# Kernel optimization log

Measured on AMD Instinct MI355X. Metric: run time of the kernel, lower is better.

The kernel has to match this reference:

```python
import jax, jax.numpy as jnp
import numpy as np

N_NODES = 100000
N_EDGES = 1600000
N_GRAPHS = 2048
IN0 = 33
H = 100
NUM_TASKS = 1
BN_EPS = 1e-5


def _gcn_layer(x, W, b, row, col, norm, n):
    # x: [N, Cin] -> [N, Cout]; GCNConv: symmetric-normalized aggregation of x @ W, plus bias
    xw = x @ W                                   # [N, Cout]
    msg = xw[row] * norm[:, None]                # [E+N, Cout] gathered + scaled messages
    out = jax.ops.segment_sum(msg, col, num_segments=n)
    return out + b


def _bn_eval(h, gamma, beta, mean, var):
    return (h - mean) * jax.lax.rsqrt(var + BN_EPS) * gamma + beta


def setup_inputs() -> dict:
    key = jax.random.key(0)
    ks = jax.random.split(key, 16)
    x = jax.random.normal(ks[0], (N_NODES, IN0), dtype=jnp.float32)
    edge_index = jax.random.randint(ks[1], (2, N_EDGES), 0, N_NODES, dtype=jnp.int64)
    batch = jnp.sort(jax.random.randint(ks[2], (N_NODES,), 0, N_GRAPHS, dtype=jnp.int64))
    # Xavier-uniform linear weights (as in _initialize_weights), zero biases
    def xav(k, fan_in, fan_out):
        lim = np.sqrt(6.0 / (fan_in + fan_out))
        return jax.random.uniform(k, (fan_in, fan_out), jnp.float32, -lim, lim)
    W0 = xav(ks[3], IN0, H)                      # layer 0: 33 -> 100
    Ws = jnp.stack([xav(ks[4 + i], H, H) for i in range(3)])  # layers 1..3: 100 -> 100
    biases = jnp.zeros((4, H), jnp.float32)
    gamma = 1.0 + 0.1 * jax.random.normal(ks[7], (4, H), jnp.float32)
    beta = 0.1 * jax.random.normal(ks[8], (4, H), jnp.float32)
    bn_mean = 0.1 * jax.random.normal(ks[9], (4, H), jnp.float32)
    bn_var = 1.0 + 0.1 * jax.random.uniform(ks[10], (4, H), jnp.float32)
    head_W = xav(ks[11], H, NUM_TASKS)
    head_b = jnp.zeros((NUM_TASKS,), jnp.float32)
    return {"x": x, "edge_index": edge_index, "batch": batch, "W0": W0, "Ws": Ws,
            "biases": biases, "gamma": gamma, "beta": beta, "bn_mean": bn_mean,
            "bn_var": bn_var, "head_W": head_W, "head_b": head_b}


def reference(x, edge_index, batch, W0, Ws, biases, gamma, beta, bn_mean, bn_var, head_W, head_b):
    n = x.shape[0]
    loop = jnp.arange(n, dtype=edge_index.dtype)
    row = jnp.concatenate([edge_index[0], loop])     # sources (+ self loops)
    col = jnp.concatenate([edge_index[1], loop])     # destinations (+ self loops)
    deg = jax.ops.segment_sum(jnp.ones_like(col, dtype=x.dtype), col, num_segments=n)
    dis = jnp.where(deg > 0, jax.lax.rsqrt(jnp.maximum(deg, 1.0)), 0.0)
    norm = dis[row] * dis[col]                       # [E+N] symmetric GCN normalization
    h = x
    for l in range(4):
        W = W0 if l == 0 else Ws[l - 1]
        h = _gcn_layer(h, W, biases[l], row, col, norm, n)
        h = _bn_eval(h, gamma[l], beta[l], bn_mean[l], bn_var[l])
        if l < 3:
            h = jax.nn.relu(h)
        # dropout: identity in eval mode
    g = jax.ops.segment_sum(h, batch, num_segments=N_GRAPHS)  # global_add_pool [G, H]
    out = g @ head_W + head_b
    return jnp.where(out >= 0, out, 0.1 * out)       # LeakyReLU(0.1)
```

## Files before the change

kernel.cpp:

```cpp
#include <hip/hip_runtime.h>
#include <hip/hip_fp16.h>

#define H100 100
#define BN_EPS 1e-5f
#define MAXD 64

typedef _Float16 h2t __attribute__((ext_vector_type(2)));

__device__ __forceinline__ float dot2f(h2t a, h2t b, float c) {
#if defined(__has_builtin) && __has_builtin(__builtin_amdgcn_fdot2)
    return __builtin_amdgcn_fdot2(a, b, c, false);
#else
    return c + (float)a.x * (float)b.x + (float)a.y * (float)b.y;
#endif
}

__device__ __forceinline__ float4 h4tof4(const uint2 u) {
    const __half2 h0 = *reinterpret_cast<const __half2*>(&u.x);
    const __half2 h1 = *reinterpret_cast<const __half2*>(&u.y);
    const float2 f0 = __half22float2(h0);
    const float2 f1 = __half22float2(h1);
    return make_float4(f0.x, f0.y, f1.x, f1.y);
}
__device__ __forceinline__ uint2 f4toh4(const float4 v) {
    __half2 h0 = __float22half2_rn(make_float2(v.x, v.y));
    __half2 h1 = __float22half2_rn(make_float2(v.z, v.w));
    uint2 u;
    u.x = *reinterpret_cast<const unsigned int*>(&h0);
    u.y = *reinterpret_cast<const unsigned int*>(&h1);
    return u;
}
__device__ __forceinline__ void f4p(float4& a, const float4 b) {
    a.x += b.x; a.y += b.y; a.z += b.z; a.w += b.w;
}

__global__ __launch_bounds__(256) void init_kernel(
    int* __restrict__ cnt, int n, int nbc,
    const float* __restrict__ b, const float* __restrict__ gamma,
    const float* __restrict__ beta, const float* __restrict__ mean,
    const float* __restrict__ var, const float* __restrict__ W0,
    const float* __restrict__ Ws, const float* __restrict__ headW,
    float* __restrict__ sarr, float* __restrict__ tarr,
    h2t* __restrict__ W0p2, h2t* __restrict__ W1p2, h2t* __restrict__ W2p2,
    float* __restrict__ wp, float* __restrict__ c3,
    float* __restrict__ gacc, int G)
{
    const int t = threadIdx.x;
    if (blockIdx.x < nbc) {
        int gid = blockIdx.x * 256 + t;
        if (gid < n) cnt[gid] = 0;
        return;
    }
    if (blockIdx.x == nbc) {
        __shared__ float ws_[H100];
        const float* W3 = Ws + 2 * H100 * H100;
        for (int idx = t; idx < 4 * H100; idx += 256) {
            float s = gamma[idx] * rsqrtf(var[idx] + BN_EPS);
            sarr[idx] = s;
            tarr[idx] = (b[idx] - mean[idx]) * s + beta[idx];
        }
        __syncthreads();
        if (t < H100) ws_[t] = sarr[3 * H100 + t] * headW[t];
        __syncthreads();
        if (t < H100) {
            float acc = 0.f;
            for (int c = 0; c < H100; ++c) acc += W3[t * H100 + c] * ws_[c];
            wp[t] = acc;
        }
        if (t == 0) {
            float acc = 0.f;
            for (int c = 0; c < H100; ++c) acc += tarr[3 * H100 + c] * headW[c];
            *c3 = acc;
        }
        return;
    }
    int idx = (blockIdx.x - nbc - 1) * 256 + t;
    if (idx < 1800) {
        int k2 = idx / 100, c = idx - k2 * 100;
        int k0 = 2 * k2, k1 = 2 * k2 + 1;
        float v0 = (k0 < 33) ? W0[k0 * H100 + c] : 0.f;
        float v1 = (k1 < 33) ? W0[k1 * H100 + c] : 0.f;
        h2t p; p.x = (_Float16)v0; p.y = (_Float16)v1;
        W0p2[idx] = p;
    } else if (idx < 6800) {
        int j = idx - 1800;
        int k2 = j / 100, c = j - k2 * 100;
        h2t p;
        p.x = (_Float16)Ws[(2 * k2) * H100 + c];
        p.y = (_Float16)Ws[(2 * k2 + 1) * H100 + c];
        W1p2[j] = p;
    } else if (idx < 12000) {
        int j = idx - 6800;
        int k2 = j / 104, c = j - k2 * 104;
        const float* W2 = Ws + H100 * H100;
        h2t p; p.x = (_Float16)0.f; p.y = (_Float16)0.f;
        if (c < H100) {
            p.x = (_Float16)W2[(2 * k2) * H100 + c];
            p.y = (_Float16)W2[(2 * k2 + 1) * H100 + c];
        }
        W2p2[j] = p;
    } else {
        int g = idx - 12000;
        if (g < G) gacc[g] = 0.f;
    }
}

__global__ __launch_bounds__(256) void fill_kernel(
    const int* __restrict__ row, const int* __restrict__ col,
    int* __restrict__ cnt, int* __restrict__ srcidx, int E)
{
    const int e0 = blockIdx.x * 2048 + threadIdx.x;
    int c[8], r[8], s[8];
    bool v[8];
    #pragma unroll
    for (int k = 0; k < 8; ++k) {
        const int e = e0 + k * 256;
        v[k] = (e < E);
        c[k] = v[k] ? col[e] : 0;
        r[k] = v[k] ? row[e] : 0;
    }
    #pragma unroll
    for (int k = 0; k < 8; ++k)
        if (v[k]) s[k] = atomicAdd(&cnt[c[k]], 1);
    #pragma unroll
    for (int k = 0; k < 8; ++k)
        if (v[k] && s[k] < MAXD) srcidx[(size_t)c[k] * MAXD + s[k]] = r[k];
}

__global__ __launch_bounds__(256) void dis_kernel(const int* __restrict__ cnt,
                                                  float* __restrict__ dis, int n) {
    int gid = blockIdx.x * 256 + threadIdx.x;
    if (gid < n) dis[gid] = rsqrtf((float)(cnt[gid] + 1));
}

__global__ __launch_bounds__(256) void xpad_kernel(
    const float* __restrict__ x, const float* __restrict__ dis,
    uint2* __restrict__ xts, int n)
{
    int tt = blockIdx.x * 256 + threadIdx.x;
    int node = tt / 9;
    if (node >= n) return;
    int q = tt - node * 9;
    const float dn = dis[node];
    float v[4];
    #pragma unroll
    for (int j = 0; j < 4; ++j) {
        int c = q * 4 + j;
        v[j] = (c < 33) ? x[node * 33 + c] * dn : 0.f;
    }
    xts[node * 9 + q] = f4toh4(make_float4(v[0], v[1], v[2], v[3]));
}

__global__ __launch_bounds__(256) void gather33_kernel(
    const int* __restrict__ cnt, const int* __restrict__ srcidx,
    const uint2* __restrict__ xts, const float* __restrict__ dis,
    float4* __restrict__ agg0, int n)
{
    const int t = blockIdx.x * 256 + threadIdx.x;
    const int node = t / 9;
    if (node >= n) return;
    const int q = t - node * 9;
    const float dn = dis[node];
    const int* __restrict__ sp = srcidx + (size_t)node * MAXD;
    const int kd = min(cnt[node], MAXD);

    float4 a0 = h4tof4(xts[node * 9 + q]);
    float4 a1 = make_float4(0.f, 0.f, 0.f, 0.f);
    int i = 0;
    for (; i + 3 < kd; i += 4) {
        const uint2 u0 = xts[sp[i] * 9 + q];
        const uint2 u1 = xts[sp[i + 1] * 9 + q];
        const uint2 u2 = xts[sp[i + 2] * 9 + q];
        const uint2 u3 = xts[sp[i + 3] * 9 + q];
        f4p(a0, h4tof4(u0)); f4p(a1, h4tof4(u1));
        f4p(a0, h4tof4(u2)); f4p(a1, h4tof4(u3));
    }
    for (; i < kd; ++i) f4p(a1, h4tof4(xts[sp[i] * 9 + q]));
    agg0[node * 9 + q] = make_float4((a0.x + a1.x) * dn, (a0.y + a1.y) * dn,
                                     (a0.z + a1.z) * dn, (a0.w + a1.w) * dn);
}

__global__ __launch_bounds__(256) void gemm_fused36_kernel(
    const float* __restrict__ agg0,
    const h2t* __restrict__ W0p2, const h2t* __restrict__ W1p2,
    const float* __restrict__ dis,
    const float* __restrict__ sarr0, const float* __restrict__ tarr0,
    uint2* __restrict__ z1h, int n)
{
    __shared__ h2t Wl[50 * H100];
    __shared__ h2t Uh[50 * 68];
    const int tid = threadIdx.x;
    const int node0 = blockIdx.x * 64;

    for (int idx = tid; idx < 64 * 18; idx += 256) {
        int r = idx / 18;
        int k2 = idx - r * 18;
        int node = node0 + r;
        h2t p; p.x = (_Float16)0.f; p.y = (_Float16)0.f;
        if (node < n) {
            const float2 ag = *reinterpret_cast<const float2*>(&agg0[node * 36 + 2 * k2]);
            p.x = (_Float16)ag.x; p.y = (_Float16)ag.y;
        }
        Uh[k2 * 68 + r] = p;
    }
    for (int idx = tid; idx < 450; idx += 256)
        reinterpret_cast<uint4*>(Wl)[idx] = reinterpret_cast<const uint4*>(W0p2)[idx];
    __syncthreads();

    const int tx = tid & 15;
    const int ty = tid >> 4;
    float acc0[4][4] = {{0.f}};
    float acc1[4][4] = {{0.f}};

    #pragma unroll 3
    for (int k2 = 0; k2 < 18; ++k2) {
        const uint4 av = *reinterpret_cast<const uint4*>(&Uh[k2 * 68 + ty * 4]);
        const h2t* a2 = reinterpret_cast<const h2t*>(&av);
        const uint4 w0v = *reinterpret_cast<const uint4*>(&Wl[k2 * H100 + tx * 4]);
        const h2t* w0 = reinterpret_cast<const h2t*>(&w0v);
        #pragma unroll
        for (int ni = 0; ni < 4; ++ni)
            #pragma unroll
            for (int ci = 0; ci < 4; ++ci)
                acc0[ni][ci] = dot2f(a2[ni], w0[ci], acc0[ni][ci]);
        if (tx < 9) {
            const uint4 w1v = *reinterpret_cast<const uint4*>(&Wl[k2 * H100 + 64 + tx * 4]);
            const h2t* w1 = reinterpret_cast<const h2t*>(&w1v);
            #pragma unroll
            for (int ni = 0; ni < 4; ++ni)
                #pragma unroll
                for (int ci = 0; ci < 4; ++ci)
                    acc1[ni][ci] = dot2f(a2[ni], w1[ci], acc1[ni][ci]);
        }
    }
    __syncthreads();

    {
        const float4 s0 = *reinterpret_cast<const float4*>(&sarr0[tx * 4]);
        const float4 t0 = *reinterpret_cast<const float4*>(&tarr0[tx * 4]);
        #pragma unroll
        for (int ni = 0; ni < 4; ++ni) {
            const int r = ty * 4 + ni;
            float h0 = fmaxf(acc0[ni][0] * s0.x + t0.x, 0.f);
            float h1 = fmaxf(acc0[ni][1] * s0.y + t0.y, 0.f);
            float hh2 = fmaxf(acc0[ni][2] * s0.z + t0.z, 0.f);
            float h3 = fmaxf(acc0[ni][3] * s0.w + t0.w, 0.f);
            h2t p0; p0.x = (_Float16)h0; p0.y = (_Float16)h1;
            h2t p1; p1.x = (_Float16)hh2; p1.y = (_Float16)h3;
            Uh[(tx * 2) * 68 + r] = p0;
            Uh[(tx * 2 + 1) * 68 + r] = p1;
        }
        if (tx < 9) {
            const float4 s1 = *reinterpret_cast<const float4*>(&sarr0[64 + tx * 4]);
            const float4 t1 = *reinterpret_cast<const float4*>(&tarr0[64 + tx * 4]);
            #pragma unroll
            for (int ni = 0; ni < 4; ++ni) {
                const int r = ty * 4 + ni;
                float h0 = fmaxf(acc1[ni][0] * s1.x + t1.x, 0.f);
                float h1 = fmaxf(acc1[ni][1] * s1.y + t1.y, 0.f);
                float hh2 = fmaxf(acc1[ni][2] * s1.z + t1.z, 0.f);
                float h3 = fmaxf(acc1[ni][3] * s1.w + t1.w, 0.f);
                h2t p0; p0.x = (_Float16)h0; p0.y = (_Float16)h1;
                h2t p1; p1.x = (_Float16)hh2; p1.y = (_Float16)h3;
                Uh[(32 + tx * 2) * 68 + r] = p0;
                Uh[(32 + tx * 2 + 1) * 68 + r] = p1;
            }
        }
    }
    for (int idx = tid; idx < 1250; idx += 256)
        reinterpret_cast<uint4*>(Wl)[idx] = reinterpret_cast<const uint4*>(W1p2)[idx];
    __syncthreads();

    float bcc0[4][4] = {{0.f}};
    float bcc1[4][4] = {{0.f}};
    #pragma unroll 5
    for (int k2 = 0; k2 < 50; ++k2) {
        const uint4 av = *reinterpret_cast<const uint4*>(&Uh[k2 * 68 + ty * 4]);
        const h2t* a2 = reinterpret_cast<const h2t*>(&av);
        const uint4 w0v = *reinterpret_cast<const uint4*>(&Wl[k2 * H100 + tx * 4]);
        const h2t* w0 = reinterpret_cast<const h2t*>(&w0v);
        #pragma unroll
        for (int ni = 0; ni < 4; ++ni)
            #pragma unroll
            for (int ci = 0; ci < 4; ++ci)
                bcc0[ni][ci] = dot2f(a2[ni], w0[ci], bcc0[ni][ci]);
        if (tx < 9) {
            const uint4 w1v = *reinterpret_cast<const uint4*>(&Wl[k2 * H100 + 64 + tx * 4]);
            const h2t* w1 = reinterpret_cast<const h2t*>(&w1v);
            #pragma unroll
            for (int ni = 0; ni < 4; ++ni)
                #pragma unroll
                for (int ci = 0; ci < 4; ++ci)
                    bcc1[ni][ci] = dot2f(a2[ni], w1[ci], bcc1[ni][ci]);
        }
    }

    #pragma unroll
    for (int ni = 0; ni < 4; ++ni) {
        const int node = node0 + ty * 4 + ni;
        if (node >= n) continue;
        const float d = dis[node];
        z1h[node * 25 + tx] = f4toh4(make_float4(
            bcc0[ni][0] * d, bcc0[ni][1] * d, bcc0[ni][2] * d, bcc0[ni][3] * d));
        if (tx < 9)
            z1h[node * 25 + 16 + tx] = f4toh4(make_float4(
                bcc1[ni][0] * d, bcc1[ni][1] * d, bcc1[ni][2] * d, bcc1[ni][3] * d));
    }
}

__global__ __launch_bounds__(512) void gather_gemm_kernel(
    const int* __restrict__ cnt, const int* __restrict__ srcidx,
    const uint2* __restrict__ z4, const float* __restrict__ dis,
    const float* __restrict__ sarr, const float* __restrict__ tarr,
    const h2t* __restrict__ W2p2, uint2* __restrict__ z2h, int n)
{
    __shared__ h2t Wl[50 * 104];
    __shared__ h2t hrow[20 * 52];
    const int tid = threadIdx.x;

    const int g = tid / 25;
    const int q = tid - g * 25;
    const bool act = (g < 20);
    const int node = blockIdx.x * 20 + g;
    const bool valid = act && (node < n);

    float4 a0 = make_float4(0.f, 0.f, 0.f, 0.f);
    float4 a1 = make_float4(0.f, 0.f, 0.f, 0.f);
    float dn = 0.f;
    if (valid) {
        a0 = h4tof4(z4[node * 25 + q]);
        dn = dis[node];
        const int* __restrict__ sp = srcidx + (size_t)node * MAXD;
        const int kd = min(cnt[node], MAXD);
        int i = 0;
        for (; i + 7 < kd; i += 8) {
            const uint2 u0 = z4[sp[i] * 25 + q];
            const uint2 u1 = z4[sp[i + 1] * 25 + q];
            const uint2 u2 = z4[sp[i + 2] * 25 + q];
            const uint2 u3 = z4[sp[i + 3] * 25 + q];
            const uint2 u4 = z4[sp[i + 4] * 25 + q];
            const uint2 u5 = z4[sp[i + 5] * 25 + q];
            const uint2 u6 = z4[sp[i + 6] * 25 + q];
            const uint2 u7 = z4[sp[i + 7] * 25 + q];
            f4p(a0, h4tof4(u0)); f4p(a1, h4tof4(u1));
            f4p(a0, h4tof4(u2)); f4p(a1, h4tof4(u3));
            f4p(a0, h4tof4(u4)); f4p(a1, h4tof4(u5));
            f4p(a0, h4tof4(u6)); f4p(a1, h4tof4(u7));
        }
        for (; i + 3 < kd; i += 4) {
            const uint2 u0 = z4[sp[i] * 25 + q];
            const uint2 u1 = z4[sp[i + 1] * 25 + q];
            const uint2 u2 = z4[sp[i + 2] * 25 + q];
            const uint2 u3 = z4[sp[i + 3] * 25 + q];
            f4p(a0, h4tof4(u0)); f4p(a1, h4tof4(u1));
            f4p(a0, h4tof4(u2)); f4p(a1, h4tof4(u3));
        }
        for (; i < kd; ++i) f4p(a1, h4tof4(z4[sp[i] * 25 + q]));
    }

    if (act) {
        const float4 s  = *reinterpret_cast<const float4*>(&sarr[q * 4]);
        const float4 tt = *reinterpret_cast<const float4*>(&tarr[q * 4]);
        float h0 = fmaxf((a0.x + a1.x) * dn * s.x + tt.x, 0.f);
        float h1 = fmaxf((a0.y + a1.y) * dn * s.y + tt.y, 0.f);
        float hh2 = fmaxf((a0.z + a1.z) * dn * s.z + tt.z, 0.f);
        float h3 = fmaxf((a0.w + a1.w) * dn * s.w + tt.w, 0.f);
        h2t p0; p0.x = (_Float16)h0; p0.y = (_Float16)h1;
        h2t p1; p1.x = (_Float16)hh2; p1.y = (_Float16)h3;
        hrow[g * 52 + q * 2]     = p0;
        hrow[g * 52 + q * 2 + 1] = p1;
    }

    for (int idx = tid; idx < 1300; idx += 512)
        reinterpret_cast<uint4*>(Wl)[idx] = reinterpret_cast<const uint4*>(W2p2)[idx];
    __syncthreads();

    if (valid) {
        float z0 = 0.f, zz1 = 0.f, z2v = 0.f, z3 = 0.f;
        const h2t* hp = &hrow[g * 52];
        #pragma unroll 5
        for (int k2 = 0; k2 < 50; ++k2) {
            const uint4 wv = *reinterpret_cast<const uint4*>(&Wl[k2 * 104 + q * 4]);
            const h2t* wh = reinterpret_cast<const h2t*>(&wv);
            const h2t hv = hp[k2];
            z0  = dot2f(hv, wh[0], z0);
            zz1 = dot2f(hv, wh[1], zz1);
            z2v = dot2f(hv, wh[2], z2v);
            z3  = dot2f(hv, wh[3], z3);
        }
        z2h[node * 25 + q] = f4toh4(make_float4(z0 * dn, zz1 * dn, z2v * dn, z3 * dn));
    }
}

__global__ __launch_bounds__(256) void gather100_head_kernel(
    const int* __restrict__ cnt, const int* __restrict__ srcidx,
    const uint2* __restrict__ z4, const float* __restrict__ dis,
    const float* __restrict__ sarr, const float* __restrict__ tarr,
    const float* __restrict__ wp, float* __restrict__ y, int n)
{
    const int tid = threadIdx.x;
    const int node = blockIdx.x * 10 + tid / 25;
    const int q = tid % 25;
    const bool valid = (tid < 250) && (node < n);

    float4 a0 = make_float4(0.f, 0.f, 0.f, 0.f);
    float4 a1 = make_float4(0.f, 0.f, 0.f, 0.f);
    float dn = 0.f;
    if (valid) {
        a0 = h4tof4(z4[node * 25 + q]);
        dn = dis[node];
        const int* __restrict__ sp = srcidx + (size_t)node * MAXD;
        const int kd = min(cnt[node], MAXD);
        int i = 0;
        for (; i + 7 < kd; i += 8) {
            const uint2 u0 = z4[sp[i] * 25 + q];
            const uint2 u1 = z4[sp[i + 1] * 25 + q];
            const uint2 u2 = z4[sp[i + 2] * 25 + q];
            const uint2 u3 = z4[sp[i + 3] * 25 + q];
            const uint2 u4 = z4[sp[i + 4] * 25 + q];
            const uint2 u5 = z4[sp[i + 5] * 25 + q];
            const uint2 u6 = z4[sp[i + 6] * 25 + q];
            const uint2 u7 = z4[sp[i + 7] * 25 + q];
            f4p(a0, h4tof4(u0)); f4p(a1, h4tof4(u1));
            f4p(a0, h4tof4(u2)); f4p(a1, h4tof4(u3));
            f4p(a0, h4tof4(u4)); f4p(a1, h4tof4(u5));
            f4p(a0, h4tof4(u6)); f4p(a1, h4tof4(u7));
        }
        for (; i + 3 < kd; i += 4) {
            const uint2 u0 = z4[sp[i] * 25 + q];
            const uint2 u1 = z4[sp[i + 1] * 25 + q];
            const uint2 u2 = z4[sp[i + 2] * 25 + q];
            const uint2 u3 = z4[sp[i + 3] * 25 + q];
            f4p(a0, h4tof4(u0)); f4p(a1, h4tof4(u1));
            f4p(a0, h4tof4(u2)); f4p(a1, h4tof4(u3));
        }
        for (; i < kd; ++i) f4p(a1, h4tof4(z4[sp[i] * 25 + q]));
    }

    const float4 s  = *reinterpret_cast<const float4*>(&sarr[q * 4]);
    const float4 tt = *reinterpret_cast<const float4*>(&tarr[q * 4]);
    const float4 w  = *reinterpret_cast<const float4*>(&wp[q * 4]);
    float hv0 = fmaxf((a0.x + a1.x) * dn * s.x + tt.x, 0.f);
    float hv1 = fmaxf((a0.y + a1.y) * dn * s.y + tt.y, 0.f);
    float hv2 = fmaxf((a0.z + a1.z) * dn * s.z + tt.z, 0.f);
    float hv3 = fmaxf((a0.w + a1.w) * dn * s.w + tt.w, 0.f);
    float partial = hv0 * w.x + hv1 * w.y + hv2 * w.z + hv3 * w.w;

    __shared__ float red[256];
    red[tid] = valid ? partial : 0.f;
    __syncthreads();
    if (valid && q == 0) {
        float sum = 0.f;
        #pragma unroll
        for (int j = 0; j < 25; ++j) sum += red[tid + j];
        y[node] = sum * dn;
    }
}

__global__ __launch_bounds__(256) void gather_scalar_kernel(
    const int* __restrict__ cnt, const int* __restrict__ srcidx,
    const float* __restrict__ y, const float* __restrict__ dis,
    const float* __restrict__ c3, const int* __restrict__ batch,
    float* __restrict__ gacc, int n)
{
    const int node = blockIdx.x * 256 + threadIdx.x;
    if (node >= n) return;
    float acc = y[node];
    float accb = 0.f;
    const int* __restrict__ sp = srcidx + (size_t)node * MAXD;
    const int kd = min(cnt[node], MAXD);
    int i = 0;
    for (; i + 7 < kd; i += 8) {
        acc  += (y[sp[i]]     + y[sp[i + 1]]) + (y[sp[i + 2]] + y[sp[i + 3]]);
        accb += (y[sp[i + 4]] + y[sp[i + 5]]) + (y[sp[i + 6]] + y[sp[i + 7]]);
    }
    for (; i + 3 < kd; i += 4)
        acc += (y[sp[i]] + y[sp[i + 1]]) + (y[sp[i + 2]] + y[sp[i + 3]]);
    for (; i < kd; ++i) acc += y[sp[i]];
    unsafeAtomicAdd(&gacc[batch[node]], dis[node] * (acc + accb) + c3[0]);
}

__global__ __launch_bounds__(256) void finish_kernel(const float* __restrict__ gacc,
                                                     const float* __restrict__ hb,
                                                     float* __restrict__ out, int G) {
    int g = blockIdx.x * 256 + threadIdx.x;
    if (g >= G) return;
    float o = gacc[g] + hb[0];
    out[g] = (o >= 0.f) ? o : 0.1f * o;
}

extern "C" void kernel_launch(void* const* d_in, const int* in_sizes, int n_in,
                              void* d_out, int out_size, void* d_ws, size_t ws_size,
                              hipStream_t stream) {
    const float* x       = (const float*)d_in[0];
    const int*   ei      = (const int*)d_in[1];
    const int*   batch   = (const int*)d_in[2];
    const float* W0      = (const float*)d_in[3];
    const float* Ws      = (const float*)d_in[4];
    const float* biases  = (const float*)d_in[5];
    const float* gamma   = (const float*)d_in[6];
    const float* beta    = (const float*)d_in[7];
    const float* bn_mean = (const float*)d_in[8];
    const float* bn_var  = (const float*)d_in[9];
    const float* headW   = (const float*)d_in[10];
    const float* headb   = (const float*)d_in[11];
    float* out = (float*)d_out;

    const int N = in_sizes[2];
    const int E = in_sizes[1] / 2;
    const int G = out_size;
    const int* row  = ei;
    const int* colp = ei + E;

    char* ws = (char*)d_ws;
    size_t off = 0;
    auto carve = [&](size_t bytes) -> void* {
        void* p = (void*)(ws + off);
        off += (bytes + 255) & ~(size_t)255;
        return p;
    };
    float*  dis    = (float*)carve((size_t)N * 4);
    uint2*  xts    = (uint2*)carve((size_t)N * 9 * 8);
    float4* agg0   = (float4*)carve((size_t)N * 9 * 16);
    uint2*  bufA   = (uint2*)carve((size_t)N * 25 * 8);
    uint2*  bufB   = (uint2*)carve((size_t)N * 25 * 8);
    float*  y      = (float*)carve((size_t)N * 4);
    int*    cnt    = (int*)carve((size_t)N * 4);
    int*    srcidx = (int*)carve((size_t)N * MAXD * 4);
    float*  sarr   = (float*)carve(4 * H100 * 4);
    float*  tarr   = (float*)carve(4 * H100 * 4);
    float*  wp     = (float*)carve(H100 * 4);
    float*  c3     = (float*)carve(256);
    h2t*    W0p2   = (h2t*)carve(1800 * 4);
    h2t*    W1p2   = (h2t*)carve(5000 * 4);
    h2t*    W2p2   = (h2t*)carve(5200 * 4);
    float*  gacc   = (float*)carve((size_t)G * 4);

    const int nb_n   = (N + 255) / 256;
    const int nb_g   = (N + 63) / 64;
    const int nb_9   = (N * 9 + 255) / 256;
    const int nb_ga  = (N + 9) / 10;
    const int nb_gg  = (N + 19) / 20;
    const int nb_f   = (E + 2047) / 2048;
    const int nb_pad = (12000 + G + 255) / 256;

    init_kernel<<<nb_n + 1 + nb_pad, 256, 0, stream>>>(
        cnt, N, nb_n,
        biases, gamma, beta, bn_mean, bn_var, W0,
        Ws, headW, sarr, tarr, W0p2, W1p2, W2p2, wp, c3, gacc, G);
    fill_kernel<<<nb_f, 256, 0, stream>>>(row, colp, cnt, srcidx, E);
    dis_kernel<<<nb_n, 256, 0, stream>>>(cnt, dis, N);
    xpad_kernel<<<nb_9, 256, 0, stream>>>(x, dis, xts, N);

    gather33_kernel<<<nb_9, 256, 0, stream>>>(cnt, srcidx, xts, dis, agg0, N);
    gemm_fused36_kernel<<<nb_g, 256, 0, stream>>>((const float*)agg0, W0p2, W1p2, dis,
                                                  sarr, tarr, bufA, N);

    gather_gemm_kernel<<<nb_gg, 512, 0, stream>>>(cnt, srcidx, bufA, dis,
                                                  sarr + H100, tarr + H100,
                                                  W2p2, bufB, N);

    gather100_head_kernel<<<nb_ga, 256, 0, stream>>>(cnt, srcidx, bufB, dis,
                                                     sarr + 2 * H100, tarr + 2 * H100, wp, y, N);

    gather_scalar_kernel<<<nb_n, 256, 0, stream>>>(cnt, srcidx, y, dis, c3, batch, gacc, N);
    finish_kernel<<<(G + 255) / 256, 256, 0, stream>>>(gacc, headb, out, G);
}
```

Measured before the change: 450.0 us.

## Build CSR adjacency via two-pass bucketed binning with shared-memory atomics

```diff
diff --git a/kernel.cpp b/kernel.cpp
--- a/kernel.cpp
+++ b/kernel.cpp
@@ -4,6 +4,8 @@
 #define H100 100
 #define BN_EPS 1e-5f
 #define MAXD 64
+#define CSR_CAP 5120
+#define NB_MAX 1024
 
 typedef _Float16 h2t __attribute__((ext_vector_type(2)));
 
@@ -35,7 +37,6 @@
 }
 
 __global__ __launch_bounds__(256) void init_kernel(
-    int* __restrict__ cnt, int n, int nbc,
     const float* __restrict__ b, const float* __restrict__ gamma,
     const float* __restrict__ beta, const float* __restrict__ mean,
     const float* __restrict__ var, const float* __restrict__ W0,
@@ -43,15 +44,11 @@
     float* __restrict__ sarr, float* __restrict__ tarr,
     h2t* __restrict__ W0p2, h2t* __restrict__ W1p2, h2t* __restrict__ W2p2,
     float* __restrict__ wp, float* __restrict__ c3,
-    float* __restrict__ gacc, int G)
+    float* __restrict__ gacc, int G,
+    int* __restrict__ bucketCnt, int NB)
 {
     const int t = threadIdx.x;
-    if (blockIdx.x < nbc) {
-        int gid = blockIdx.x * 256 + t;
-        if (gid < n) cnt[gid] = 0;
-        return;
-    }
-    if (blockIdx.x == nbc) {
+    if (blockIdx.x == 0) {
         __shared__ float ws_[H100];
         const float* W3 = Ws + 2 * H100 * H100;
         for (int idx = t; idx < 4 * H100; idx += 256) {
@@ -74,7 +71,7 @@
         }
         return;
     }
-    int idx = (blockIdx.x - nbc - 1) * 256 + t;
+    int idx = (blockIdx.x - 1) * 256 + t;
     if (idx < 1800) {
         int k2 = idx / 100, c = idx - k2 * 100;
         int k0 = 2 * k2, k1 = 2 * k2 + 1;
@@ -102,35 +99,78 @@
     } else {
         int g = idx - 12000;
         if (g < G) gacc[g] = 0.f;
-    }
-}
-
-__global__ __launch_bounds__(256) void fill_kernel(
+        else if (g - G < NB) bucketCnt[g - G] = 0;
+    }
+}
+
+__global__ __launch_bounds__(512) void csr_p1_kernel(
     const int* __restrict__ row, const int* __restrict__ col,
-    int* __restrict__ cnt, int* __restrict__ srcidx, int E)
-{
-    const int e0 = blockIdx.x * 2048 + threadIdx.x;
-    int c[8], r[8], s[8];
+    int* __restrict__ bucketCnt, unsigned int* __restrict__ bucketBuf,
+    int E, int NB)
+{
+    __shared__ int hcnt[NB_MAX];
+    __shared__ int hbase[NB_MAX];
+    const int tid = threadIdx.x;
+    for (int j = tid; j < NB; j += 512) hcnt[j] = 0;
+    __syncthreads();
+
+    const int e0 = blockIdx.x * 4096 + tid;
+    int bk[8], rk[8];
+    unsigned int pv[8];
     bool v[8];
     #pragma unroll
     for (int k = 0; k < 8; ++k) {
-        const int e = e0 + k * 256;
+        const int e = e0 + k * 512;
         v[k] = (e < E);
-        c[k] = v[k] ? col[e] : 0;
-        r[k] = v[k] ? row[e] : 0;
-    }
+        const int c = v[k] ? col[e] : 0;
+        const int r = v[k] ? row[e] : 0;
+        bk[k] = c >> 8;
+        pv[k] = (unsigned int)r | ((unsigned int)(c & 255) << 24);
+        if (v[k]) rk[k] = atomicAdd(&hcnt[bk[k]], 1);
+    }
+    __syncthreads();
+    for (int j = tid; j < NB; j += 512)
+        if (hcnt[j] > 0) hbase[j] = atomicAdd(&bucketCnt[j], hcnt[j]);
+    __syncthreads();
     #pragma unroll
-    for (int k = 0; k < 8; ++k)
-        if (v[k]) s[k] = atomicAdd(&cnt[c[k]], 1);
-    #pragma unroll
-    for (int k = 0; k < 8; ++k)
-        if (v[k] && s[k] < MAXD) srcidx[(size_t)c[k] * MAXD + s[k]] = r[k];
-}
-
-__global__ __launch_bounds__(256) void dis_kernel(const int* __restrict__ cnt,
-                                                  float* __restrict__ dis, int n) {
-    int gid = blockIdx.x * 256 + threadIdx.x;
-    if (gid < n) dis[gid] = rsqrtf((float)(cnt[gid] + 1));
+    for (int k = 0; k < 8; ++k) {
+        if (v[k]) {
+            const int pos = hbase[bk[k]] + rk[k];
+            if (pos < CSR_CAP)
+                bucketBuf[(size_t)bk[k] * CSR_CAP + pos] = pv[k];
+        }
+    }
+}
+
+__global__ __launch_bounds__(512) void csr_p2_kernel(
+    const int* __restrict__ bucketCnt, const unsigned int* __restrict__ bucketBuf,
+    int* __restrict__ cnt, float* __restrict__ dis, int* __restrict__ srcidx,
+    int n)
+{
+    __shared__ int lcnt[256];
+    const int b = blockIdx.x;
+    const int tid = threadIdx.x;
+    if (tid < 256) lcnt[tid] = 0;
+    __syncthreads();
+    const int cb = min(bucketCnt[b], CSR_CAP);
+    const unsigned int* __restrict__ bp = bucketBuf + (size_t)b * CSR_CAP;
+    const int node0 = b << 8;
+    for (int pos = tid; pos < cb; pos += 512) {
+        const unsigned int v = bp[pos];
+        const int d = (int)(v >> 24);
+        const int r = (int)(v & 0xFFFFFFu);
+        const int s = atomicAdd(&lcnt[d], 1);
+        if (s < MAXD) srcidx[(size_t)(node0 + d) * MAXD + s] = r;
+    }
+    __syncthreads();
+    if (tid < 256) {
+        const int node = node0 + tid;
+        if (node < n) {
+            const int c = lcnt[tid];
+            cnt[node] = c;
+            dis[node] = rsqrtf((float)(c + 1));
+        }
+    }
 }
 
 __global__ __launch_bounds__(256) void xpad_kernel(
@@ -536,20 +576,25 @@
     h2t*    W2p2   = (h2t*)carve(5200 * 4);
     float*  gacc   = (float*)carve((size_t)G * 4);
 
+    const int NB = (N + 255) >> 8;
+    unsigned int* bucketBuf = (unsigned int*)carve((size_t)NB * CSR_CAP * 4);
+    int*          bucketCnt = (int*)carve((size_t)NB * 4);
+
     const int nb_n   = (N + 255) / 256;
     const int nb_g   = (N + 63) / 64;
     const int nb_9   = (N * 9 + 255) / 256;
     const int nb_ga  = (N + 9) / 10;
     const int nb_gg  = (N + 19) / 20;
-    const int nb_f   = (E + 2047) / 2048;
-    const int nb_pad = (12000 + G + 255) / 256;
-
-    init_kernel<<<nb_n + 1 + nb_pad, 256, 0, stream>>>(
-        cnt, N, nb_n,
+    const int nb_p1  = (E + 4095) / 4096;
+    const int nb_pad = (12000 + G + NB + 255) / 256;
+
+    init_kernel<<<1 + nb_pad, 256, 0, stream>>>(
         biases, gamma, beta, bn_mean, bn_var, W0,
-        Ws, headW, sarr, tarr, W0p2, W1p2, W2p2, wp, c3, gacc, G);
-    fill_kernel<<<nb_f, 256, 0, stream>>>(row, colp, cnt, srcidx, E);
-    dis_kernel<<<nb_n, 256, 0, stream>>>(cnt, dis, N);
+        Ws, headW, sarr, tarr, W0p2, W1p2, W2p2, wp, c3, gacc, G, bucketCnt, NB);
+
+    csr_p1_kernel<<<nb_p1, 512, 0, stream>>>(row, colp, bucketCnt, bucketBuf, E, NB);
+    csr_p2_kernel<<<NB, 512, 0, stream>>>(bucketCnt, bucketBuf, cnt, dis, srcidx, N);
+
     xpad_kernel<<<nb_9, 256, 0, stream>>>(x, dis, xts, N);
 
     gather33_kernel<<<nb_9, 256, 0, stream>>>(cnt, srcidx, xts, dis, agg0, N);
```

Measured after the change: 387.6 us. 13.9% less time.
